# Performance work log

Hardware: AMD Instinct MI355X
Metric: run time of the kernel (lower is better)

Reference implementation:

```python
import jax, jax.numpy as jnp
import numpy as np

N, IN_DIM, OUT_DIM, HEADS = 50000, 256, 256, 8
C = OUT_DIM // HEADS  # per-head channels = 32
E = 800000
G = 64  # number of graphs in the batch
NEG_SLOPE = 0.2
GN_EPS = 1e-5


def setup_inputs() -> dict:
    key = jax.random.key(0)
    ks = jax.random.split(key, 12)
    x = jax.random.normal(ks[0], (N, IN_DIM), dtype=jnp.float32)
    edge_index = jax.random.randint(ks[1], (2, E), 0, N, dtype=jnp.int64)
    batch = jnp.sort(jax.random.randint(ks[2], (N,), 0, G, dtype=jnp.int64))
    s = 1.0 / np.sqrt(IN_DIM)
    W_l = jax.random.uniform(ks[3], (IN_DIM, HEADS * C), jnp.float32, -s, s)
    b_l = jnp.zeros((HEADS * C,), jnp.float32)
    W_r = jax.random.uniform(ks[4], (IN_DIM, HEADS * C), jnp.float32, -s, s)
    b_r = jnp.zeros((HEADS * C,), jnp.float32)
    att = jax.random.normal(ks[5], (HEADS, C), dtype=jnp.float32) / np.sqrt(C)
    bias = jnp.zeros((HEADS * C,), jnp.float32)
    gn_weight = jnp.ones((OUT_DIM,), jnp.float32)
    gn_bias = jnp.zeros((OUT_DIM,), jnp.float32)
    gn_mean_scale = jnp.ones((OUT_DIM,), jnp.float32)
    return {"x": x, "edge_index": edge_index, "batch": batch,
            "W_l": W_l, "b_l": b_l, "W_r": W_r, "b_r": b_r,
            "att": att, "bias": bias, "gn_weight": gn_weight,
            "gn_bias": gn_bias, "gn_mean_scale": gn_mean_scale}


def _gat_block(x, src, dst, batch, W_l, b_l, W_r, b_r, att, bias,
               gn_weight, gn_bias, gn_mean_scale):
    n = x.shape[0]
    # GATv2Conv (add_self_loops=True, concat=True)
    loops = jnp.arange(n, dtype=src.dtype)
    src = jnp.concatenate([src, loops])
    dst = jnp.concatenate([dst, loops])
    xl = (x @ W_l + b_l).reshape(n, HEADS, C)  # source transform
    xr = (x @ W_r + b_r).reshape(n, HEADS, C)  # target transform
    e = jax.nn.leaky_relu(xl[src] + xr[dst], NEG_SLOPE)  # [E', H, C]
    logits = jnp.einsum('ehc,hc->eh', e, att)            # [E', H]
    # segment softmax over incoming edges of each destination node
    m = jax.ops.segment_max(logits, dst, num_segments=n)
    alpha = jnp.exp(logits - m[dst])
    denom = jax.ops.segment_sum(alpha, dst, num_segments=n)
    alpha = alpha / (denom[dst] + 1e-16)
    msg = xl[src] * alpha[:, :, None]                    # [E', H, C]
    h = jax.ops.segment_sum(msg, dst, num_segments=n).reshape(n, HEADS * C) + bias
    # identity residual (in_dim == out_dim) + ELU
    h = jax.nn.elu(h + x)
    # GraphNorm (post-norm)
    counts = jnp.maximum(jax.ops.segment_sum(jnp.ones((n,), h.dtype), batch,
                                             num_segments=G), 1.0)
    mean = jax.ops.segment_sum(h, batch, num_segments=G) / counts[:, None]
    out0 = h - gn_mean_scale * mean[batch]
    var = jax.ops.segment_sum(out0 * out0, batch, num_segments=G) / counts[:, None]
    return gn_weight * out0 / jnp.sqrt(var[batch] + GN_EPS) + gn_bias


def reference(x, edge_index, batch, W_l, b_l, W_r, b_r, att, bias,
              gn_weight, gn_bias, gn_mean_scale):
    return _gat_block(x, edge_index[0], edge_index[1], batch,
                      W_l, b_l, W_r, b_r, att, bias,
                      gn_weight, gn_bias, gn_mean_scale)
```

## Files before the change

kernel.cpp:

```cpp
#include <hip/hip_runtime.h>
#include <hip/hip_bf16.h>
#include <stdint.h>

#define N_NODES 50000
#define MPAD    50048
#define IN_DIM  256
#define EDGES   800000
#define EPRIME  (EDGES + N_NODES)
#define NGRAPH  64
#define GN_EPS  1e-5f
#define ECPAD   53248
#define HIST_BLOCKS 3321
#define PREP_BLOCKS 512
#define MSG_SPLIT 4
#define MSG_RANGE (N_NODES / MSG_SPLIT)

typedef __attribute__((ext_vector_type(8))) short short8;
typedef __attribute__((ext_vector_type(4))) float floatx4;
typedef __attribute__((ext_vector_type(2))) float float2v;

__device__ __forceinline__ uint32_t pk2bf(float a, float b) {
    union { __hip_bfloat162 h; uint32_t u; } cv;
    cv.h = __float22bfloat162_rn(make_float2(a, b));
    return cv.u;
}

__device__ __forceinline__ unsigned short f2b(float f) {
    uint32_t u = __float_as_uint(f);
    u += 0x7fffu + ((u >> 16) & 1u);
    return (unsigned short)(u >> 16);
}

__device__ __forceinline__ float2v up2(uint32_t u) {
    float2v r;
    r[0] = __uint_as_float(u << 16);
    r[1] = __uint_as_float(u & 0xffff0000u);
    return r;
}

__global__ __launch_bounds__(256) void k_pre(const float* __restrict__ Wl,
                                             const float* __restrict__ Wr,
                                             unsigned short* __restrict__ Wt,
                                             const int* __restrict__ ei,
                                             const int* __restrict__ batch,
                                             int* __restrict__ ecount,
                                             int* __restrict__ ncount,
                                             int* __restrict__ sedge) {
    if (blockIdx.x < PREP_BLOCKS) {
        int idx = blockIdx.x * 256 + threadIdx.x;
        int n = idx >> 8, k = idx & 255;
        float v = (n < 256) ? Wl[k * 256 + n] : Wr[k * 256 + (n - 256)];
        Wt[idx] = f2b(v);
        return;
    }
    __shared__ int hist[NGRAPH];
    if (threadIdx.x < NGRAPH) hist[threadIdx.x] = 0;
    __syncthreads();
    int e = (blockIdx.x - PREP_BLOCKS) * 256 + threadIdx.x;
    if (e < EPRIME) {
        int d = (e < EDGES) ? ei[EDGES + e] : (e - EDGES);
        atomicAdd(&ecount[d], 1);
    }
    if (e < N_NODES) atomicAdd(&hist[batch[e]], 1);
    if (blockIdx.x == PREP_BLOCKS && threadIdx.x < 192) sedge[EPRIME + threadIdx.x] = 0;
    __syncthreads();
    if (threadIdx.x < NGRAPH && hist[threadIdx.x])
        atomicAdd(&ncount[threadIdx.x], hist[threadIdx.x]);
}

__global__ __launch_bounds__(512) void k_gemm(const float* __restrict__ x,
                                              const unsigned short* __restrict__ Wt,
                                              const float* __restrict__ bl,
                                              const float* __restrict__ br,
                                              unsigned short* __restrict__ XL,
                                              unsigned short* __restrict__ XR) {
    __shared__ unsigned short As[64 * 256];
    int rbase = blockIdx.x * 64;
    int tid = threadIdx.x;

#pragma unroll
    for (int it = 0; it < 4; ++it) {
        int c = it * 512 + tid;
        int row = c >> 5, ch = c & 31;
        int gr = rbase + row;
        float4 f0, f1;
        if (gr < N_NODES) {
            const float4* src = (const float4*)(x + (size_t)gr * 256 + ch * 8);
            f0 = src[0]; f1 = src[1];
        } else {
            f0 = make_float4(0.f,0.f,0.f,0.f); f1 = f0;
        }
        uint32_t p0 = pk2bf(f0.x, f0.y), p1 = pk2bf(f0.z, f0.w);
        uint32_t p2 = pk2bf(f1.x, f1.y), p3 = pk2bf(f1.z, f1.w);
        uint4 hv = make_uint4(p0, p1, p2, p3);
        *(uint4*)(As + row * 256 + (ch ^ (row & 7)) * 8) = hv;
    }
    __syncthreads();

    int w = tid >> 6;
    int l = tid & 63;
    int m = l & 15, q = l >> 4;

    floatx4 acc[4][4];
#pragma unroll
    for (int rf = 0; rf < 4; ++rf)
#pragma unroll
        for (int cf = 0; cf < 4; ++cf)
            acc[rf][cf] = (floatx4){0.f, 0.f, 0.f, 0.f};

    const unsigned short* wbase = Wt + (size_t)(w * 64) * 256;

#pragma unroll
    for (int kk = 0; kk < 8; ++kk) {
        short8 a[4];
#pragma unroll
        for (int rf = 0; rf < 4; ++rf) {
            int row = rf * 16 + m;
            int ch = (kk * 4 + q) ^ (row & 7);
            a[rf] = *(const short8*)(As + row * 256 + ch * 8);
        }
#pragma unroll
        for (int cf = 0; cf < 4; ++cf) {
            short8 b = *(const short8*)(wbase + (size_t)(cf * 16 + m) * 256 + kk * 32 + q * 8);
#pragma unroll
            for (int rf = 0; rf < 4; ++rf)
                acc[rf][cf] = __builtin_amdgcn_mfma_f32_16x16x32_bf16(b, a[rf], acc[rf][cf], 0, 0, 0);
        }
    }

    unsigned short* obase = (w < 4) ? XL : XR;
    const float* bptr = (w < 4) ? bl : br;
    int cb = (w & 3) * 64;
#pragma unroll
    for (int cf = 0; cf < 4; ++cf) {
        int chb = cb + cf * 16 + q * 4;
        float4 bv = *(const float4*)(bptr + chb);
#pragma unroll
        for (int rf = 0; rf < 4; ++rf) {
            int node = rbase + rf * 16 + m;
            uint2 o;
            o.x = pk2bf(acc[rf][cf][0] + bv.x, acc[rf][cf][1] + bv.y);
            o.y = pk2bf(acc[rf][cf][2] + bv.z, acc[rf][cf][3] + bv.w);
            *(uint2*)(obase + (size_t)node * 256 + chb) = o;
        }
    }
}

__global__ __launch_bounds__(1024) void k_scan_all(const int* __restrict__ ecount,
                                                   int* __restrict__ estart,
                                                   int* __restrict__ ecursor) {
    __shared__ int wsum[16];
    int t = threadIdx.x, w = t >> 6, l = t & 63;
    int carry = 0;
    for (int base = 0; base < ECPAD; base += 4096) {
        int4 v = ((const int4*)(ecount + base))[t];
        int s = v.x + v.y + v.z + v.w;
        int sc = s;
#pragma unroll
        for (int off = 1; off < 64; off <<= 1) {
            int n = __shfl_up(sc, off);
            sc += (l >= off) ? n : 0;
        }
        if (l == 63) wsum[w] = sc;
        __syncthreads();
        int woff = 0, ctot = 0;
#pragma unroll
        for (int i = 0; i < 16; ++i) {
            int wi = wsum[i];
            woff += (i < w) ? wi : 0;
            ctot += wi;
        }
        int e0 = carry + woff + (sc - s);
        int4 o;
        o.x = e0; o.y = e0 + v.x; o.z = o.y + v.y; o.w = o.z + v.z;
        ((int4*)(estart  + base))[t] = o;
        ((int4*)(ecursor + base))[t] = o;
        carry += ctot;
        __syncthreads();
    }
}

__global__ __launch_bounds__(256) void k_scatter(const int* __restrict__ ei,
                                                 int* __restrict__ ecursor,
                                                 int* __restrict__ sedge) {
    int e = blockIdx.x * 256 + threadIdx.x;
    if (e >= EPRIME) return;
    int s, d;
    if (e < EDGES) { s = ei[e]; d = ei[EDGES + e]; }
    else           { s = d = e - EDGES; }
    int pos = atomicAdd(&ecursor[d], 1);
    sedge[pos] = s;
}

__global__ __launch_bounds__(256) void k_msg(const unsigned short* __restrict__ XL,
                                             const unsigned short* __restrict__ XRb,
                                             const float* __restrict__ x,
                                             const float* __restrict__ att,
                                             const float* __restrict__ bias,
                                             const int* __restrict__ sedge,
                                             const int* __restrict__ estart,
                                             const int* __restrict__ ecount,
                                             float* __restrict__ out,
                                             int lo) {
    int d = lo + (int)((blockIdx.x * 256 + threadIdx.x) >> 6);
    int l = threadIdx.x & 63;
    int lofs = l * 8;

    float4 xin  = ((const float4*)(x + (size_t)d * 256))[l];
    float4 bvv  = ((const float4*)bias)[l];
    float4 attv = ((const float4*)att)[l];
    float2v a601 = {0.6f * attv.x, 0.6f * attv.y};
    float2v a623 = {0.6f * attv.z, 0.6f * attv.w};
    float a40 = 0.4f * attv.x, a41 = 0.4f * attv.y;
    float a42 = 0.4f * attv.z, a43 = 0.4f * attv.w;

    uint2 xru = ((const uint2*)(XRb + (size_t)d * 256))[l];
    float2v xr01 = up2(xru.x), xr23 = up2(xru.y);

    int s0  = __builtin_amdgcn_readfirstlane(estart[d]);
    int cnt = __builtin_amdgcn_readfirstlane(ecount[d]);

    auto ldrow = [&](int src) -> uint2 {
        size_t off = ((size_t)(uint32_t)__builtin_amdgcn_readfirstlane(src)) << 9;
        return *(const uint2*)((const char*)XL + off + lofs);
    };

    float den0 = 0.f, den1 = 0.f, den2 = 0.f, den3 = 0.f;
    float2v A01 = {0.f,0.f}, A23 = {0.f,0.f};
    float2v B01 = {0.f,0.f}, B23 = {0.f,0.f};
    float2v C01 = {0.f,0.f}, C23 = {0.f,0.f};
    float2v D01 = {0.f,0.f}, D23 = {0.f,0.f};

    auto proc = [&](uint2 U, float& den, float2v& R01, float2v& R23) {
        float2v x01 = up2(U.x), x23 = up2(U.y);
        float2v z01 = x01 + xr01, z23 = x23 + xr23;
        float2v q = z01 * a601 + z23 * a623;
        float t0 = fmaf(fabsf(z01[0]), a40, q[0]);
        float t1 = fmaf(fabsf(z01[1]), a41, q[1]);
        t0 = fmaf(fabsf(z23[0]), a42, t0);
        t1 = fmaf(fabsf(z23[1]), a43, t1);
        float pp = t0 + t1;
        int pi = __float_as_int(pp);
        pp += __int_as_float(__builtin_amdgcn_update_dpp(0, pi, 0xB1, 0xF, 0xF, true));
        pi = __float_as_int(pp);
        pp += __int_as_float(__builtin_amdgcn_update_dpp(0, pi, 0x4E, 0xF, 0xF, true));
        pi = __float_as_int(pp);
        pp += __int_as_float(__builtin_amdgcn_update_dpp(0, pi, 0x141, 0xF, 0xF, true));
        float al = __expf(fminf(pp, 80.f));
        den += al;
        float2v al2 = {al, al};
        R01 += al2 * x01;
        R23 += al2 * x23;
    };

    uint2 P0 = ldrow(sedge[s0]);
    uint2 P1 = ldrow(sedge[s0 + 1]);
    uint2 P2 = ldrow(sedge[s0 + 2]);
    uint2 P3 = ldrow(sedge[s0 + 3]);

    int nq = cnt >> 2;
    for (int qq = 0; qq < nq; ++qq) {
        uint2 Q0 = P0, Q1 = P1, Q2 = P2, Q3 = P3;
        int nb = s0 + (qq + 1) * 4;
        P0 = ldrow(sedge[nb]);
        P1 = ldrow(sedge[nb + 1]);
        P2 = ldrow(sedge[nb + 2]);
        P3 = ldrow(sedge[nb + 3]);
        proc(Q0, den0, A01, A23);
        proc(Q1, den1, B01, B23);
        proc(Q2, den2, C01, C23);
        proc(Q3, den3, D01, D23);
    }
    int rem = cnt & 3;
    if (rem > 0) proc(P0, den0, A01, A23);
    if (rem > 1) proc(P1, den1, B01, B23);
    if (rem > 2) proc(P2, den2, C01, C23);

    float inv = 1.f / ((den0 + den1) + (den2 + den3) + 1e-16f);
    A01 = (A01 + B01) + (C01 + D01);
    A23 = (A23 + B23) + (C23 + D23);

    float h0 = A01[0] * inv + bvv.x + xin.x; h0 = (h0 > 0.f) ? h0 : (__expf(h0) - 1.f);
    float h1 = A01[1] * inv + bvv.y + xin.y; h1 = (h1 > 0.f) ? h1 : (__expf(h1) - 1.f);
    float h2 = A23[0] * inv + bvv.z + xin.z; h2 = (h2 > 0.f) ? h2 : (__expf(h2) - 1.f);
    float h3 = A23[1] * inv + bvv.w + xin.w; h3 = (h3 > 0.f) ? h3 : (__expf(h3) - 1.f);
    ((float4*)(out + (size_t)d * 256))[l] = make_float4(h0, h1, h2, h3);
}

#define GN_ROWS 64
__global__ __launch_bounds__(256) void k_gn_sum(const float* __restrict__ h,
                                                const int* __restrict__ batch,
                                                float* __restrict__ gsum,
                                                float* __restrict__ gsq) {
    __shared__ int bsh[GN_ROWS];
    __shared__ float4 redS[4][64];
    __shared__ float4 redQ[4][64];
    int r0 = blockIdx.x * GN_ROWS;
    int t = threadIdx.x;
    if (t < GN_ROWS) {
        int i = r0 + t;
        bsh[t] = (i < N_NODES) ? batch[i] : -2;
    }
    __syncthreads();
    int l = t & 63, w = t >> 6;
    bool uni = (r0 + GN_ROWS <= N_NODES) && (bsh[0] == bsh[GN_ROWS - 1]);

    if (uni) {
        const float* hp = h + (size_t)(r0 + w) * 256 + l * 4;
        float4 s1 = make_float4(0.f, 0.f, 0.f, 0.f);
        float4 s2 = make_float4(0.f, 0.f, 0.f, 0.f);
#pragma unroll
        for (int k = 0; k < 16; ++k) {
            float4 v = *(const float4*)(hp + (size_t)k * 1024);
            s1.x += v.x; s1.y += v.y; s1.z += v.z; s1.w += v.w;
            s2.x = fmaf(v.x, v.x, s2.x);
            s2.y = fmaf(v.y, v.y, s2.y);
            s2.z = fmaf(v.z, v.z, s2.z);
            s2.w = fmaf(v.w, v.w, s2.w);
        }
        redS[w][l] = s1; redQ[w][l] = s2;
        __syncthreads();
        if (w == 0) {
            float4 b1 = redS[1][l], c1 = redS[2][l], d1 = redS[3][l];
            float4 b2 = redQ[1][l], c2 = redQ[2][l], d2 = redQ[3][l];
            s1.x += b1.x + c1.x + d1.x; s1.y += b1.y + c1.y + d1.y;
            s1.z += b1.z + c1.z + d1.z; s1.w += b1.w + c1.w + d1.w;
            s2.x += b2.x + c2.x + d2.x; s2.y += b2.y + c2.y + d2.y;
            s2.z += b2.z + c2.z + d2.z; s2.w += b2.w + c2.w + d2.w;
            int g = bsh[0];
            float* gp = gsum + g * 256 + l * 4;
            atomicAdd(gp + 0, s1.x); atomicAdd(gp + 1, s1.y);
            atomicAdd(gp + 2, s1.z); atomicAdd(gp + 3, s1.w);
            float* gq = gsq + g * 256 + l * 4;
            atomicAdd(gq + 0, s2.x); atomicAdd(gq + 1, s2.y);
            atomicAdd(gq + 2, s2.z); atomicAdd(gq + 3, s2.w);
        }
        return;
    }

    float4 s1 = make_float4(0.f, 0.f, 0.f, 0.f);
    float4 s2 = make_float4(0.f, 0.f, 0.f, 0.f);
    int g = (r0 + w < N_NODES) ? bsh[w] : -1;
    for (int j = w; j < GN_ROWS; j += 4) {
        int ii = r0 + j;
        if (ii >= N_NODES) break;
        int bg = bsh[j];
        if (bg != g) {
            float* gp = gsum + g * 256 + l * 4;
            atomicAdd(gp + 0, s1.x); atomicAdd(gp + 1, s1.y);
            atomicAdd(gp + 2, s1.z); atomicAdd(gp + 3, s1.w);
            float* gq = gsq + g * 256 + l * 4;
            atomicAdd(gq + 0, s2.x); atomicAdd(gq + 1, s2.y);
            atomicAdd(gq + 2, s2.z); atomicAdd(gq + 3, s2.w);
            s1 = make_float4(0.f, 0.f, 0.f, 0.f);
            s2 = make_float4(0.f, 0.f, 0.f, 0.f);
            g = bg;
        }
        float4 v = *(const float4*)(h + (size_t)ii * 256 + l * 4);
        s1.x += v.x; s1.y += v.y; s1.z += v.z; s1.w += v.w;
        s2.x = fmaf(v.x, v.x, s2.x);
        s2.y = fmaf(v.y, v.y, s2.y);
        s2.z = fmaf(v.z, v.z, s2.z);
        s2.w = fmaf(v.w, v.w, s2.w);
    }
    if (g >= 0) {
        float* gp = gsum + g * 256 + l * 4;
        atomicAdd(gp + 0, s1.x); atomicAdd(gp + 1, s1.y);
        atomicAdd(gp + 2, s1.z); atomicAdd(gp + 3, s1.w);
        float* gq = gsq + g * 256 + l * 4;
        atomicAdd(gq + 0, s2.x); atomicAdd(gq + 1, s2.y);
        atomicAdd(gq + 2, s2.z); atomicAdd(gq + 3, s2.w);
    }
}

#define FIN_BLOCKS 2048
__global__ __launch_bounds__(256) void k_final(float* __restrict__ out,
                                               const int* __restrict__ batch,
                                               const float* __restrict__ gsum,
                                               const float* __restrict__ gsq,
                                               const int* __restrict__ ncount,
                                               const float* __restrict__ gnw,
                                               const float* __restrict__ gnb,
                                               const float* __restrict__ gms) {
    int l = threadIdx.x & 63, wr = threadIdx.x >> 6;
    float4 wv = ((const float4*)gnw)[l];
    float4 bv = ((const float4*)gnb)[l];
    float4 sv = ((const float4*)gms)[l];
    for (int i = blockIdx.x * 4 + wr; i < N_NODES; i += FIN_BLOCKS * 4) {
        int g = batch[i];
        float inv = 1.f / fmaxf((float)ncount[g], 1.f);
        float4 hv = ((const float4*)(out + (size_t)i * 256))[l];
        float4 ms = ((const float4*)(gsum + g * 256))[l];
        float4 qs = ((const float4*)(gsq  + g * 256))[l];
        float4 o;
        {
            float m = ms.x * inv, q = qs.x * inv;
            o.x = wv.x * (hv.x - sv.x * m) * rsqrtf(q - m * m * sv.x * (2.f - sv.x) + GN_EPS) + bv.x;
        }
        {
            float m = ms.y * inv, q = qs.y * inv;
            o.y = wv.y * (hv.y - sv.y * m) * rsqrtf(q - m * m * sv.y * (2.f - sv.y) + GN_EPS) + bv.y;
        }
        {
            float m = ms.z * inv, q = qs.z * inv;
            o.z = wv.z * (hv.z - sv.z * m) * rsqrtf(q - m * m * sv.z * (2.f - sv.z) + GN_EPS) + bv.z;
        }
        {
            float m = ms.w * inv, q = qs.w * inv;
            o.w = wv.w * (hv.w - sv.w * m) * rsqrtf(q - m * m * sv.w * (2.f - sv.w) + GN_EPS) + bv.w;
        }
        ((float4*)(out + (size_t)i * 256))[l] = o;
    }
}

extern "C" void kernel_launch(void* const* d_in, const int* in_sizes, int n_in,
                              void* d_out, int out_size, void* d_ws, size_t ws_size,
                              hipStream_t stream) {
    const float* x    = (const float*)d_in[0];
    const int*   ei   = (const int*)d_in[1];
    const int*   batch= (const int*)d_in[2];
    const float* Wl   = (const float*)d_in[3];
    const float* bl   = (const float*)d_in[4];
    const float* Wr   = (const float*)d_in[5];
    const float* br   = (const float*)d_in[6];
    const float* att  = (const float*)d_in[7];
    const float* bias = (const float*)d_in[8];
    const float* gnw  = (const float*)d_in[9];
    const float* gnb  = (const float*)d_in[10];
    const float* gms  = (const float*)d_in[11];
    float* out = (float*)d_out;

    char* p = (char*)d_ws;
    auto alloc = [&](size_t bytes) -> char* {
        char* r = p;
        p += (bytes + 255) & ~(size_t)255;
        return r;
    };
    unsigned short* Wt  = (unsigned short*)alloc((size_t)512 * 256 * 2);
    unsigned short* XL  = (unsigned short*)alloc((size_t)MPAD * 256 * 2);
    unsigned short* XRb = (unsigned short*)alloc((size_t)MPAD * 256 * 2);
    int* estart         = (int*)alloc((size_t)ECPAD * 4);
    int* ecursor        = (int*)alloc((size_t)ECPAD * 4);
    int* sedge          = (int*)alloc((size_t)(EPRIME + 192) * 4);
    int* ecount         = (int*)alloc((size_t)ECPAD * 4);
    int* ncount         = (int*)alloc((size_t)NGRAPH * 4);
    float* gsum         = (float*)alloc((size_t)2 * NGRAPH * 256 * 4);
    float* gsq          = gsum + NGRAPH * 256;
    size_t zbytes = (size_t)((char*)(gsum + 2 * NGRAPH * 256) - (char*)ecount);
    hipMemsetAsync(ecount, 0, zbytes, stream);

    k_pre<<<PREP_BLOCKS + HIST_BLOCKS, 256, 0, stream>>>(Wl, Wr, Wt, ei, batch,
                                                         ecount, ncount, sedge);
    k_gemm<<<MPAD / 64, 512, 0, stream>>>(x, Wt, bl, br, XL, XRb);

    k_scan_all<<<1, 1024, 0, stream>>>(ecount, estart, ecursor);
    k_scatter<<<HIST_BLOCKS, 256, 0, stream>>>(ei, ecursor, sedge);

    for (int s = 0; s < MSG_SPLIT; ++s)
        k_msg<<<MSG_RANGE / 4, 256, 0, stream>>>(XL, XRb, x, att, bias,
                                                 sedge, estart, ecount, out,
                                                 s * MSG_RANGE);

    k_gn_sum<<<(N_NODES + GN_ROWS - 1) / GN_ROWS, 256, 0, stream>>>(out, batch, gsum, gsq);
    k_final<<<FIN_BLOCKS, 256, 0, stream>>>(out, batch, gsum, gsq,
                                            ncount, gnw, gnb, gms);
}
```

Before: 391.4 us.

## Pre-swizzle weights into MFMA fragment order, merge msg launches, double per-thread work

The weight-transpose prep now writes the bf16 weights directly in MFMA B-fragment order, so each lane in the GEMM loads one contiguous 16-byte chunk and the wavefront reads a contiguous block instead of strided rows. The histogram and scatter kernels each process two edges per thread over half as many blocks. The four split message-passing launches become a single launch over all nodes. Together these cut launch overhead and uncoalesced weight loads, at the cost of a more complex index mapping in the prep kernel.

```diff
diff --git a/kernel.cpp b/kernel.cpp
--- a/kernel.cpp
+++ b/kernel.cpp
@@ -10,10 +10,8 @@
 #define NGRAPH  64
 #define GN_EPS  1e-5f
 #define ECPAD   53248
-#define HIST_BLOCKS 3321
 #define PREP_BLOCKS 512
-#define MSG_SPLIT 4
-#define MSG_RANGE (N_NODES / MSG_SPLIT)
+#define HISTB   1661
 
 typedef __attribute__((ext_vector_type(8))) short short8;
 typedef __attribute__((ext_vector_type(4))) float floatx4;
@@ -47,21 +45,27 @@
                                              int* __restrict__ ncount,
                                              int* __restrict__ sedge) {
     if (blockIdx.x < PREP_BLOCKS) {
-        int idx = blockIdx.x * 256 + threadIdx.x;
-        int n = idx >> 8, k = idx & 255;
+        int n = blockIdx.x;
+        int k = threadIdx.x;
         float v = (n < 256) ? Wl[k * 256 + n] : Wr[k * 256 + (n - 256)];
-        Wt[idx] = f2b(v);
+        int g = n >> 4, m = n & 15;
+        int kk = k >> 5, q = (k >> 3) & 3, e = k & 7;
+        Wt[(((g * 8 + kk) * 64) + q * 16 + m) * 8 + e] = f2b(v);
         return;
     }
     __shared__ int hist[NGRAPH];
     if (threadIdx.x < NGRAPH) hist[threadIdx.x] = 0;
     __syncthreads();
-    int e = (blockIdx.x - PREP_BLOCKS) * 256 + threadIdx.x;
-    if (e < EPRIME) {
-        int d = (e < EDGES) ? ei[EDGES + e] : (e - EDGES);
-        atomicAdd(&ecount[d], 1);
-    }
-    if (e < N_NODES) atomicAdd(&hist[batch[e]], 1);
+    int base = (blockIdx.x - PREP_BLOCKS) * 512 + threadIdx.x;
+#pragma unroll
+    for (int off = 0; off < 512; off += 256) {
+        int e = base + off;
+        if (e < EPRIME) {
+            int d = (e < EDGES) ? ei[EDGES + e] : (e - EDGES);
+            atomicAdd(&ecount[d], 1);
+        }
+        if (e < N_NODES) atomicAdd(&hist[batch[e]], 1);
+    }
     if (blockIdx.x == PREP_BLOCKS && threadIdx.x < 192) sedge[EPRIME + threadIdx.x] = 0;
     __syncthreads();
     if (threadIdx.x < NGRAPH && hist[threadIdx.x])
@@ -108,8 +112,6 @@
         for (int cf = 0; cf < 4; ++cf)
             acc[rf][cf] = (floatx4){0.f, 0.f, 0.f, 0.f};
 
-    const unsigned short* wbase = Wt + (size_t)(w * 64) * 256;
-
 #pragma unroll
     for (int kk = 0; kk < 8; ++kk) {
         short8 a[4];
@@ -121,7 +123,7 @@
         }
 #pragma unroll
         for (int cf = 0; cf < 4; ++cf) {
-            short8 b = *(const short8*)(wbase + (size_t)(cf * 16 + m) * 256 + kk * 32 + q * 8);
+            short8 b = *(const short8*)(Wt + ((((w * 4 + cf) * 8 + kk) * 64) + l) * 8);
 #pragma unroll
             for (int rf = 0; rf < 4; ++rf)
                 acc[rf][cf] = __builtin_amdgcn_mfma_f32_16x16x32_bf16(b, a[rf], acc[rf][cf], 0, 0, 0);
@@ -183,13 +185,18 @@
 __global__ __launch_bounds__(256) void k_scatter(const int* __restrict__ ei,
                                                  int* __restrict__ ecursor,
                                                  int* __restrict__ sedge) {
-    int e = blockIdx.x * 256 + threadIdx.x;
-    if (e >= EPRIME) return;
-    int s, d;
-    if (e < EDGES) { s = ei[e]; d = ei[EDGES + e]; }
-    else           { s = d = e - EDGES; }
-    int pos = atomicAdd(&ecursor[d], 1);
-    sedge[pos] = s;
+    int base = blockIdx.x * 512 + threadIdx.x;
+#pragma unroll
+    for (int off = 0; off < 512; off += 256) {
+        int e = base + off;
+        if (e < EPRIME) {
+            int s, d;
+            if (e < EDGES) { s = ei[e]; d = ei[EDGES + e]; }
+            else           { s = d = e - EDGES; }
+            int pos = atomicAdd(&ecursor[d], 1);
+            sedge[pos] = s;
+        }
+    }
 }
 
 __global__ __launch_bounds__(256) void k_msg(const unsigned short* __restrict__ XL,
@@ -200,9 +207,8 @@
                                              const int* __restrict__ sedge,
                                              const int* __restrict__ estart,
                                              const int* __restrict__ ecount,
-                                             float* __restrict__ out,
-                                             int lo) {
-    int d = lo + (int)((blockIdx.x * 256 + threadIdx.x) >> 6);
+                                             float* __restrict__ out) {
+    int d = (int)((blockIdx.x * 256 + threadIdx.x) >> 6);
     int l = threadIdx.x & 63;
     int lofs = l * 8;
 
@@ -449,17 +455,15 @@
     size_t zbytes = (size_t)((char*)(gsum + 2 * NGRAPH * 256) - (char*)ecount);
     hipMemsetAsync(ecount, 0, zbytes, stream);
 
-    k_pre<<<PREP_BLOCKS + HIST_BLOCKS, 256, 0, stream>>>(Wl, Wr, Wt, ei, batch,
-                                                         ecount, ncount, sedge);
+    k_pre<<<PREP_BLOCKS + HISTB, 256, 0, stream>>>(Wl, Wr, Wt, ei, batch,
+                                                   ecount, ncount, sedge);
     k_gemm<<<MPAD / 64, 512, 0, stream>>>(x, Wt, bl, br, XL, XRb);
 
     k_scan_all<<<1, 1024, 0, stream>>>(ecount, estart, ecursor);
-    k_scatter<<<HIST_BLOCKS, 256, 0, stream>>>(ei, ecursor, sedge);
-
-    for (int s = 0; s < MSG_SPLIT; ++s)
-        k_msg<<<MSG_RANGE / 4, 256, 0, stream>>>(XL, XRb, x, att, bias,
-                                                 sedge, estart, ecount, out,
-                                                 s * MSG_RANGE);
+    k_scatter<<<HISTB, 256, 0, stream>>>(ei, ecursor, sedge);
+
+    k_msg<<<N_NODES / 4, 256, 0, stream>>>(XL, XRb, x, att, bias,
+                                           sedge, estart, ecount, out);
 
     k_gn_sum<<<(N_NODES + GN_ROWS - 1) / GN_ROWS, 256, 0, stream>>>(out, batch, gsum, gsq);
     k_final<<<FIN_BLOCKS, 256, 0, stream>>>(out, batch, gsum, gsq,
```

After: 352.3 us. -10.0%, faster.
